# Performance work log

Measured on AMD Instinct MI355X. Metric: run time of the kernel, lower is better.

The kernel has to match this reference:

```python
import jax, jax.numpy as jnp
import numpy as np

B, C, H, W = 16, 512, 32, 32
G = 32          # GroupNorm groups
EPS = 1e-5      # torch GroupNorm default eps


def setup_inputs() -> dict:
    key = jax.random.key(0)
    ks = jax.random.split(key, 7)
    s = 0.02
    return {
        "x": jax.random.normal(ks[0], (B, C, H, W), jnp.float32),
        "temb": jax.random.normal(ks[1], (1, C), jnp.float32),
        "gn_scale": jnp.ones((C,), jnp.float32),
        "gn_bias": jnp.zeros((C,), jnp.float32),
        "wq": jax.random.normal(ks[2], (C, C), jnp.float32) * s,
        "bq": jnp.zeros((C,), jnp.float32),
        "wk": jax.random.normal(ks[3], (C, C), jnp.float32) * s,
        "bk": jnp.zeros((C,), jnp.float32),
        "wv": jax.random.normal(ks[4], (C, C), jnp.float32) * s,
        "bv": jnp.zeros((C,), jnp.float32),
        "wo": jax.random.normal(ks[5], (C, C), jnp.float32) * s,
        "bo": jnp.zeros((C,), jnp.float32),
    }


def _group_norm(x, scale, bias):
    b, c, h, w = x.shape
    xg = x.reshape(b, G, c // G, h, w)
    mu = xg.mean(axis=(2, 3, 4), keepdims=True)
    var = xg.var(axis=(2, 3, 4), keepdims=True)
    xn = ((xg - mu) * jax.lax.rsqrt(var + EPS)).reshape(b, c, h, w)
    return xn * scale[None, :, None, None] + bias[None, :, None, None]


def _conv1x1(x, w, b):
    # 1x1 conv == channel matmul
    return jnp.einsum('oc,bchw->bohw', w, x) + b[None, :, None, None]


def reference(x, temb, gn_scale, gn_bias, wq, bq, wk, bk, wv, bv, wo, bo):
    b, c, h, w = x.shape
    hw = h * w
    hn = _group_norm(x, gn_scale, gn_bias)
    q = _conv1x1(hn, wq, bq).reshape(b, c, hw)   # (B, C, HW)
    k = _conv1x1(hn, wk, bk).reshape(b, c, hw)
    v = _conv1x1(hn, wv, bv).reshape(b, c, hw)
    # scores over spatial positions, scaled by C^-0.5
    attn = jnp.einsum('bci,bcj->bij', q, k) * (c ** -0.5)  # (B, HW, HW)
    attn = jax.nn.softmax(attn, axis=-1)
    out = jnp.einsum('bij,bcj->bci', attn, v).reshape(b, c, h, w)
    out = _conv1x1(out, wo, bo)
    return x + out
```

## Files before the change

kernel.cpp:

```cpp
#include <hip/hip_runtime.h>

#define B_   16
#define C_   512
#define HW_  1024
#define G_   32
#define CPG  16
#define EPS  1e-5f
#define CHW  ((size_t)C_ * HW_)
#define HW2  ((size_t)HW_ * HW_)

typedef __attribute__((ext_vector_type(8))) short bf16x8;
typedef __attribute__((ext_vector_type(4))) float f32x4;

__device__ inline unsigned short f2bf(float f) {
    union { float f; unsigned u; } v; v.f = f;
    unsigned r = v.u + 0x7fffu + ((v.u >> 16) & 1u);
    return (unsigned short)(r >> 16);
}
__device__ inline float bf2f(unsigned short h) {
    union { unsigned u; float f; } v; v.u = (unsigned)h << 16;
    return v.f;
}

__device__ inline void gload_lds16(const void* g, void* lds) {
    __builtin_amdgcn_global_load_lds(
        (const __attribute__((address_space(1))) void*)g,
        (__attribute__((address_space(3))) void*)lds,
        16, 0, 0);
}

__global__ __launch_bounds__(256) void prep_kernel(
    const float* __restrict__ w0, const float* __restrict__ w1,
    const float* __restrict__ w2, const float* __restrict__ w3,
    unsigned short* __restrict__ o0, unsigned short* __restrict__ o1,
    unsigned short* __restrict__ o2, unsigned short* __restrict__ o3,
    const float* __restrict__ bq, const float* __restrict__ bk,
    float* __restrict__ bqk)
{
    int id = blockIdx.x;
    if (id < 1024) {
        int wsel = id >> 8;
        int blk  = id & 255;
        const float* in = (wsel == 0) ? w0 : (wsel == 1) ? w1 : (wsel == 2) ? w2 : w3;
        unsigned short* out = (wsel == 0) ? o0 : (wsel == 1) ? o1 : (wsel == 2) ? o2 : o3;
        int i = (blk * 256 + threadIdx.x) * 4;
        float4 f = *reinterpret_cast<const float4*>(in + i);
        ushort4 o;
        o.x = f2bf(f.x); o.y = f2bf(f.y); o.z = f2bf(f.z); o.w = f2bf(f.w);
        *reinterpret_cast<ushort4*>(out + i) = o;
    } else {
        int t = threadIdx.x;
        bqk[t]       = bq[t];
        bqk[256 + t] = bq[256 + t];
        bqk[512 + t] = bk[t];
        bqk[768 + t] = bk[256 + t];
    }
}

__global__ __launch_bounds__(256) void gn_fused(
    const float* __restrict__ x, const float* __restrict__ scale,
    const float* __restrict__ bias, unsigned short* __restrict__ hn_g)
{
    const int bg = blockIdx.x;
    const int g  = bg & 31;
    const float* xp = x + (size_t)bg * CPG * HW_;
    const int N = CPG * HW_;

    float s = 0.f, ss = 0.f;
    const float4* xv = reinterpret_cast<const float4*>(xp);
#pragma unroll
    for (int k = 0; k < 16; ++k) {
        float4 v = xv[threadIdx.x + k * 256];
        s  += v.x + v.y + v.z + v.w;
        ss += v.x * v.x + v.y * v.y + v.z * v.z + v.w * v.w;
    }
    for (int off = 32; off; off >>= 1) {
        s  += __shfl_down(s,  off, 64);
        ss += __shfl_down(ss, off, 64);
    }
    __shared__ float red0[4], red1[4];
    int lane = threadIdx.x & 63, wid = threadIdx.x >> 6;
    if (lane == 0) { red0[wid] = s; red1[wid] = ss; }
    __syncthreads();
    __shared__ float smu, sinv;
    if (threadIdx.x == 0) {
        float S  = red0[0] + red0[1] + red0[2] + red0[3];
        float SS = red1[0] + red1[1] + red1[2] + red1[3];
        float mu = S / (float)N;
        float var = SS / (float)N - mu * mu;
        smu = mu; sinv = rsqrtf(var + EPS);
    }
    __syncthreads();
    const float mu = smu, inv = sinv;

    float scl[CPG], bia[CPG];
#pragma unroll
    for (int cc = 0; cc < CPG; ++cc) {
        float sc = scale[g * CPG + cc];
        scl[cc] = sc * inv;
        bia[cc] = bias[g * CPG + cc] - mu * sc * inv;
    }

    unsigned short* dst = hn_g + (size_t)bg * 16384;
#pragma unroll
    for (int it = 0; it < 4; ++it) {
        int i = it * 256 + threadIdx.x;
        __align__(16) unsigned short y[CPG];
#pragma unroll
        for (int cc = 0; cc < CPG; ++cc)
            y[cc] = f2bf(xp[cc * HW_ + i] * scl[cc] + bia[cc]);
        unsigned short* d = dst + (size_t)i * 16;
        *reinterpret_cast<uint4*>(d)     = *reinterpret_cast<uint4*>(&y[0]);
        *reinterpret_cast<uint4*>(d + 8) = *reinterpret_cast<uint4*>(&y[8]);
    }
}

template<int OUTF32, int BIASMODE, int HASRES, int GA, int GB>
__device__ __forceinline__ void gemm_body(
    short* lds, int bx, int by, int bz,
    const short* __restrict__ A, size_t sA, int ldA,
    const short* __restrict__ Bm, size_t sB, int ldB,
    void* __restrict__ Cm, size_t sC, int ldC,
    const float* __restrict__ bias,
    const float* __restrict__ res, size_t sR,
    int K, float alpha)
{
    const short* Ab = A  + (size_t)bz * sA;
    const short* Bb = Bm + (size_t)bz * sB;
    const int m0 = by * 128;
    const int n0 = bx * 128;

    const int t = threadIdx.x;
    const int wv = t >> 6, lane = t & 63;
    const int wm = wv >> 1, wn = wv & 1;
    const int fr = lane & 15;
    const int cb = (lane >> 4) * 16;

    size_t srcA0, srcA1, srcB0, srcB1;
    {
        int p0 = t * 16;
        int a0 = p0 ^ (((p0 >> 7) & 3) << 4);
        int p1 = 4096 + t * 16;
        int a1 = p1 ^ (((p1 >> 7) & 3) << 4);
        int r0 = a0 >> 6, cs0 = (a0 & 63) >> 1;
        int r1 = a1 >> 6, cs1 = (a1 & 63) >> 1;
        if (GA) {
            int mA0 = m0 + r0, mA1 = m0 + r1;
            srcA0 = (size_t)(mA0 >> 10) * 524288 + (size_t)(cs0 >> 4) * 16384
                  + (size_t)(mA0 & 1023) * 16 + (cs0 & 15);
            srcA1 = (size_t)(mA1 >> 10) * 524288 + (size_t)(cs1 >> 4) * 16384
                  + (size_t)(mA1 & 1023) * 16 + (cs1 & 15);
        } else {
            srcA0 = (size_t)(m0 + r0) * ldA + cs0;
            srcA1 = (size_t)(m0 + r1) * ldA + cs1;
        }
        if (GB) {
            int nB0 = n0 + r0, nB1 = n0 + r1;
            srcB0 = (size_t)(nB0 >> 10) * 524288 + (size_t)(cs0 >> 4) * 16384
                  + (size_t)(nB0 & 1023) * 16 + (cs0 & 15);
            srcB1 = (size_t)(nB1 >> 10) * 524288 + (size_t)(cs1 >> 4) * 16384
                  + (size_t)(nB1 & 1023) * 16 + (cs1 & 15);
        } else {
            srcB0 = (size_t)(n0 + r0) * ldB + cs0;
            srcB1 = (size_t)(n0 + r1) * ldB + cs1;
        }
    }
    auto stageA = [&](int par, int kh, int kt_src) {
        const size_t k0 = (size_t)(kt_src * 64 + kh * 32) * (GA ? 1024 : 1);
        const short* s = Ab + k0;
        short* d = &lds[(par * 2 + kh) * 4096 + t * 8];
        gload_lds16(s + srcA0, d);
        gload_lds16(s + srcA1, d + 2048);
    };
    auto stageB = [&](int par, int kh, int kt_src) {
        const size_t k0 = (size_t)(kt_src * 64 + kh * 32) * (GB ? 1024 : 1);
        const short* s = Bb + k0;
        short* d = &lds[16384 + (par * 2 + kh) * 4096 + t * 8];
        gload_lds16(s + srcB0, d);
        gload_lds16(s + srcB1, d + 2048);
    };

    int aoffs[4], boffs[4];
#pragma unroll
    for (int fi = 0; fi < 4; ++fi) {
        int row = wm * 64 + fi * 16 + fr;
        int off = row * 64 + cb;
        aoffs[fi] = off ^ (((off >> 7) & 3) << 4);
    }
#pragma unroll
    for (int fj = 0; fj < 4; ++fj) {
        int row = wn * 64 + fj * 16 + fr;
        int off = row * 64 + cb;
        boffs[fj] = off ^ (((off >> 7) & 3) << 4);
    }

    f32x4 acc[4][4];
#pragma unroll
    for (int i = 0; i < 4; ++i)
#pragma unroll
        for (int j = 0; j < 4; ++j) acc[i][j] = (f32x4){0.f, 0.f, 0.f, 0.f};

    const int NT = K >> 6;
    const char* L = (const char*)lds;

    stageA(0, 0, 0); stageB(0, 0, 0);
    stageA(0, 1, 0); stageB(0, 1, 0);
    stageA(1, 0, 1); stageB(1, 0, 1);

    for (int kt = 0; kt < NT; ++kt) {
        const int par = kt & 1;
        const int AB0 = (par * 2) * 8192;
        const int AB1 = AB0 + 8192;
        const int BB0 = 32768 + (par * 2) * 8192;
        const int BB1 = BB0 + 8192;

        bf16x8 af0, af1, af2, af3, bf0, bf1;

        if (kt == NT - 1) asm volatile("s_waitcnt vmcnt(4)\n\ts_barrier" ::: "memory");
        else              asm volatile("s_waitcnt vmcnt(8)\n\ts_barrier" ::: "memory");
        af0 = *(const bf16x8*)(L + AB0 + aoffs[0]);
        af1 = *(const bf16x8*)(L + AB0 + aoffs[1]);
        af2 = *(const bf16x8*)(L + AB0 + aoffs[2]);
        af3 = *(const bf16x8*)(L + AB0 + aoffs[3]);
        bf0 = *(const bf16x8*)(L + BB0 + boffs[0]);
        bf1 = *(const bf16x8*)(L + BB0 + boffs[1]);
        if (kt + 1 < NT) stageA(par ^ 1, 1, kt + 1);
        __builtin_amdgcn_s_setprio(1);
        acc[0][0] = __builtin_amdgcn_mfma_f32_16x16x32_bf16(af0, bf0, acc[0][0], 0, 0, 0);
        acc[1][0] = __builtin_amdgcn_mfma_f32_16x16x32_bf16(af1, bf0, acc[1][0], 0, 0, 0);
        acc[2][0] = __builtin_amdgcn_mfma_f32_16x16x32_bf16(af2, bf0, acc[2][0], 0, 0, 0);
        acc[3][0] = __builtin_amdgcn_mfma_f32_16x16x32_bf16(af3, bf0, acc[3][0], 0, 0, 0);
        acc[0][1] = __builtin_amdgcn_mfma_f32_16x16x32_bf16(af0, bf1, acc[0][1], 0, 0, 0);
        acc[1][1] = __builtin_amdgcn_mfma_f32_16x16x32_bf16(af1, bf1, acc[1][1], 0, 0, 0);
        acc[2][1] = __builtin_amdgcn_mfma_f32_16x16x32_bf16(af2, bf1, acc[2][1], 0, 0, 0);
        acc[3][1] = __builtin_amdgcn_mfma_f32_16x16x32_bf16(af3, bf1, acc[3][1], 0, 0, 0);
        __builtin_amdgcn_s_setprio(0);
        asm volatile("s_waitcnt lgkmcnt(0)\n\ts_barrier" ::: "memory");

        bf0 = *(const bf16x8*)(L + BB0 + boffs[2]);
        bf1 = *(const bf16x8*)(L + BB0 + boffs[3]);
        if (kt + 1 < NT) stageB(par ^ 1, 1, kt + 1);
        __builtin_amdgcn_s_setprio(1);
        acc[0][2] = __builtin_amdgcn_mfma_f32_16x16x32_bf16(af0, bf0, acc[0][2], 0, 0, 0);
        acc[1][2] = __builtin_amdgcn_mfma_f32_16x16x32_bf16(af1, bf0, acc[1][2], 0, 0, 0);
        acc[2][2] = __builtin_amdgcn_mfma_f32_16x16x32_bf16(af2, bf0, acc[2][2], 0, 0, 0);
        acc[3][2] = __builtin_amdgcn_mfma_f32_16x16x32_bf16(af3, bf0, acc[3][2], 0, 0, 0);
        acc[0][3] = __builtin_amdgcn_mfma_f32_16x16x32_bf16(af0, bf1, acc[0][3], 0, 0, 0);
        acc[1][3] = __builtin_amdgcn_mfma_f32_16x16x32_bf16(af1, bf1, acc[1][3], 0, 0, 0);
        acc[2][3] = __builtin_amdgcn_mfma_f32_16x16x32_bf16(af2, bf1, acc[2][3], 0, 0, 0);
        acc[3][3] = __builtin_amdgcn_mfma_f32_16x16x32_bf16(af3, bf1, acc[3][3], 0, 0, 0);
        __builtin_amdgcn_s_setprio(0);
        asm volatile("s_waitcnt lgkmcnt(0)\n\ts_barrier" ::: "memory");

        if (kt == NT - 1) asm volatile("s_waitcnt vmcnt(0)\n\ts_barrier" ::: "memory");
        else              asm volatile("s_waitcnt vmcnt(8)\n\ts_barrier" ::: "memory");
        af0 = *(const bf16x8*)(L + AB1 + aoffs[0]);
        af1 = *(const bf16x8*)(L + AB1 + aoffs[1]);
        af2 = *(const bf16x8*)(L + AB1 + aoffs[2]);
        af3 = *(const bf16x8*)(L + AB1 + aoffs[3]);
        bf0 = *(const bf16x8*)(L + BB1 + boffs[0]);
        bf1 = *(const bf16x8*)(L + BB1 + boffs[1]);
        if (kt + 2 < NT) stageA(par, 0, kt + 2);
        __builtin_amdgcn_s_setprio(1);
        acc[0][0] = __builtin_amdgcn_mfma_f32_16x16x32_bf16(af0, bf0, acc[0][0], 0, 0, 0);
        acc[1][0] = __builtin_amdgcn_mfma_f32_16x16x32_bf16(af1, bf0, acc[1][0], 0, 0, 0);
        acc[2][0] = __builtin_amdgcn_mfma_f32_16x16x32_bf16(af2, bf0, acc[2][0], 0, 0, 0);
        acc[3][0] = __builtin_amdgcn_mfma_f32_16x16x32_bf16(af3, bf0, acc[3][0], 0, 0, 0);
        acc[0][1] = __builtin_amdgcn_mfma_f32_16x16x32_bf16(af0, bf1, acc[0][1], 0, 0, 0);
        acc[1][1] = __builtin_amdgcn_mfma_f32_16x16x32_bf16(af1, bf1, acc[1][1], 0, 0, 0);
        acc[2][1] = __builtin_amdgcn_mfma_f32_16x16x32_bf16(af2, bf1, acc[2][1], 0, 0, 0);
        acc[3][1] = __builtin_amdgcn_mfma_f32_16x16x32_bf16(af3, bf1, acc[3][1], 0, 0, 0);
        __builtin_amdgcn_s_setprio(0);
        asm volatile("s_waitcnt lgkmcnt(0)\n\ts_barrier" ::: "memory");

        bf0 = *(const bf16x8*)(L + BB1 + boffs[2]);
        bf1 = *(const bf16x8*)(L + BB1 + boffs[3]);
        if (kt + 2 < NT) stageB(par, 0, kt + 2);
        __builtin_amdgcn_s_setprio(1);
        acc[0][2] = __builtin_amdgcn_mfma_f32_16x16x32_bf16(af0, bf0, acc[0][2], 0, 0, 0);
        acc[1][2] = __builtin_amdgcn_mfma_f32_16x16x32_bf16(af1, bf0, acc[1][2], 0, 0, 0);
        acc[2][2] = __builtin_amdgcn_mfma_f32_16x16x32_bf16(af2, bf0, acc[2][2], 0, 0, 0);
        acc[3][2] = __builtin_amdgcn_mfma_f32_16x16x32_bf16(af3, bf0, acc[3][2], 0, 0, 0);
        acc[0][3] = __builtin_amdgcn_mfma_f32_16x16x32_bf16(af0, bf1, acc[0][3], 0, 0, 0);
        acc[1][3] = __builtin_amdgcn_mfma_f32_16x16x32_bf16(af1, bf1, acc[1][3], 0, 0, 0);
        acc[2][3] = __builtin_amdgcn_mfma_f32_16x16x32_bf16(af2, bf1, acc[2][3], 0, 0, 0);
        acc[3][3] = __builtin_amdgcn_mfma_f32_16x16x32_bf16(af3, bf1, acc[3][3], 0, 0, 0);
        __builtin_amdgcn_s_setprio(0);
        asm volatile("s_waitcnt lgkmcnt(0)\n\ts_barrier" ::: "memory");
    }

    const int rq = (lane >> 4) * 4;
#pragma unroll
    for (int fi = 0; fi < 4; ++fi) {
#pragma unroll
        for (int rg = 0; rg < 4; ++rg) {
            int row = m0 + wm * 64 + fi * 16 + rq + rg;
            float bm = (BIASMODE == 1) ? bias[row] : 0.f;
#pragma unroll
            for (int fj = 0; fj < 4; ++fj) {
                int col = n0 + wn * 64 + fj * 16 + fr;
                float vv = acc[fi][fj][rg] * alpha + bm;
                if (BIASMODE == 2) vv += bias[col];
                size_t off = (size_t)row * ldC + col;
                if (HASRES) vv += res[(size_t)bz * sR + off];
                if (OUTF32) ((float*)Cm)[(size_t)bz * sC + off] = vv;
                else ((unsigned short*)Cm)[(size_t)bz * sC + off] = f2bf(vv);
            }
        }
    }
}

template<int OUTF32, int BIASMODE, int HASRES, int GA, int GB>
__global__ __launch_bounds__(256) void gemm_4w(
    const short* __restrict__ A, size_t sA, int ldA,
    const short* __restrict__ Bm, size_t sB, int ldB,
    void* __restrict__ Cm, size_t sC, int ldC,
    const float* __restrict__ bias,
    const float* __restrict__ res, size_t sR,
    int K, float alpha, int lx, int ly)
{
    __shared__ __align__(16) short lds[32768];
    const int h = blockIdx.x;
    const int w = (h & 7) * ((int)gridDim.x >> 3) + (h >> 3);
    const int bx = w & ((1 << lx) - 1);
    const int by = (w >> lx) & ((1 << ly) - 1);
    const int bz = w >> (lx + ly);
    gemm_body<OUTF32, BIASMODE, HASRES, GA, GB>(
        lds, bx, by, bz, A, sA, ldA, Bm, sB, ldB, Cm, sC, ldC,
        bias, res, sR, K, alpha);
}

__global__ __launch_bounds__(256) void qkv_kernel(
    const short* __restrict__ hn_g, const short* __restrict__ wsq,
    const float* __restrict__ bqk, short* __restrict__ qk_t,
    const short* __restrict__ wsv, const float* __restrict__ bv,
    short* __restrict__ v)
{
    __shared__ __align__(16) short lds[32768];
    const int h = blockIdx.x;
    const int w = (h & 7) * 192 + (h >> 3);
    if (w < 1024) {
        gemm_body<0, 2, 0, 1, 0>(lds, w & 7, w >> 3, 0,
            hn_g, 0, 0, wsq, 0, C_, qk_t, 0, HW_, bqk, nullptr, 0, C_, 1.0f);
    } else {
        const int u = w - 1024;
        gemm_body<0, 1, 0, 0, 1>(lds, u & 7, (u >> 3) & 3, u >> 5,
            wsv, 0, C_, hn_g, CHW, 0, v, CHW, HW_, bv, nullptr, 0, C_, 1.0f);
    }
}

__global__ __launch_bounds__(256) void softmax_kernel(unsigned short* __restrict__ attn)
{
    size_t row = blockIdx.x;
    unsigned short* p = attn + row * HW_;
    ushort4 raw = reinterpret_cast<ushort4*>(p)[threadIdx.x];
    float v0 = bf2f(raw.x), v1 = bf2f(raw.y), v2 = bf2f(raw.z), v3 = bf2f(raw.w);

    float mx = fmaxf(fmaxf(v0, v1), fmaxf(v2, v3));
    for (int off = 32; off; off >>= 1) mx = fmaxf(mx, __shfl_down(mx, off, 64));
    __shared__ float redm[4], reds[4];
    int lane = threadIdx.x & 63, wid = threadIdx.x >> 6;
    if (lane == 0) redm[wid] = mx;
    __syncthreads();
    mx = fmaxf(fmaxf(redm[0], redm[1]), fmaxf(redm[2], redm[3]));

    v0 = __expf(v0 - mx); v1 = __expf(v1 - mx);
    v2 = __expf(v2 - mx); v3 = __expf(v3 - mx);
    float sum = v0 + v1 + v2 + v3;
    for (int off = 32; off; off >>= 1) sum += __shfl_down(sum, off, 64);
    if (lane == 0) reds[wid] = sum;
    __syncthreads();
    sum = reds[0] + reds[1] + reds[2] + reds[3];

    float inv = 1.f / sum;
    ushort4 o;
    o.x = f2bf(v0 * inv); o.y = f2bf(v1 * inv);
    o.z = f2bf(v2 * inv); o.w = f2bf(v3 * inv);
    reinterpret_cast<ushort4*>(p)[threadIdx.x] = o;
}

extern "C" void kernel_launch(void* const* d_in, const int* in_sizes, int n_in,
                              void* d_out, int out_size, void* d_ws, size_t ws_size,
                              hipStream_t stream)
{
    const float* x        = (const float*)d_in[0];
    const float* gn_scale = (const float*)d_in[2];
    const float* gn_bias  = (const float*)d_in[3];
    const float* wq = (const float*)d_in[4];
    const float* bq = (const float*)d_in[5];
    const float* wk = (const float*)d_in[6];
    const float* bk = (const float*)d_in[7];
    const float* wv = (const float*)d_in[8];
    const float* bv = (const float*)d_in[9];
    const float* wo = (const float*)d_in[10];
    const float* bo = (const float*)d_in[11];
    float* out = (float*)d_out;

    short* ws = (short*)d_ws;
    const size_t E = (size_t)B_ * C_ * HW_;
    short* hn_g = ws;
    short* qk_t = hn_g + E;
    short* v    = qk_t + 2 * E;
    short* ao_t = v + E;
    short* attn = ao_t + E;
    short* wsq  = attn + 2 * E;
    short* wsk  = wsq + (size_t)C_ * C_;
    short* wsv  = wsk + (size_t)C_ * C_;
    short* wso  = wsv + (size_t)C_ * C_;
    float* bqk  = (float*)(wso + (size_t)C_ * C_);

    const float inv_sqrt_c = 0.044194173824159216f;

    prep_kernel<<<dim3(1025), 256, 0, stream>>>(
        wq, wk, wv, wo,
        (unsigned short*)wsq, (unsigned short*)wsk,
        (unsigned short*)wsv, (unsigned short*)wso,
        bq, bk, bqk);

    gn_fused<<<dim3(B_ * G_), 256, 0, stream>>>(
        x, gn_scale, gn_bias, (unsigned short*)hn_g);

    qkv_kernel<<<dim3(1536), 256, 0, stream>>>(
        hn_g, wsq, bqk, qk_t, wsv, bv, v);

    gemm_4w<0, 0, 0, 0, 0><<<dim3(1024), 256, 0, stream>>>(
        qk_t, HW2, HW_, qk_t + C_, HW2, HW_, attn, HW2, HW_,
        nullptr, nullptr, 0, C_, inv_sqrt_c, 3, 3);

    softmax_kernel<<<dim3(B_ * HW_), 256, 0, stream>>>((unsigned short*)attn);

    gemm_4w<0, 0, 0, 0, 0><<<dim3(512), 256, 0, stream>>>(
        attn, HW2, HW_, v, CHW, HW_, ao_t, CHW, C_,
        nullptr, nullptr, 0, HW_, 1.0f, 2, 3);

    gemm_4w<1, 1, 1, 0, 0><<<dim3(512), 256, 0, stream>>>(
        wso, 0, C_, ao_t, CHW, C_, out, CHW, HW_, bo, x, CHW, C_,
        1.0f, 3, 2);
}
```

Before: 132.9 us.

## Fuse softmax normalization into PV GEMM A-tile load via precomputed row stats

Replaces the in-place softmax kernel with a stats-only pass that writes per-row max and inverse sum. The attention-times-V GEMM then loads raw scores into registers, applies exp and normalization, and writes bf16 to LDS, instead of staging the tile with direct global-to-LDS copies. This removes the softmax write-back of the full score matrix. In exchange the GEMM's A path now goes through registers with exp work inside the main loop, and the pipeline wait counts are retuned, which may reduce overlap.

```diff
diff --git a/kernel.cpp b/kernel.cpp
--- a/kernel.cpp
+++ b/kernel.cpp
@@ -115,7 +115,34 @@
     }
 }
 
-template<int OUTF32, int BIASMODE, int HASRES, int GA, int GB>
+__global__ __launch_bounds__(256) void row_stats(const unsigned short* __restrict__ attn,
+                                                 float2* __restrict__ rowstat)
+{
+    const int h = blockIdx.x;
+    const int row = (h & 7) * 2048 + (h >> 3);
+    const unsigned short* p = attn + (size_t)row * HW_;
+    ushort4 raw = reinterpret_cast<const ushort4*>(p)[threadIdx.x];
+    float v0 = bf2f(raw.x), v1 = bf2f(raw.y), v2 = bf2f(raw.z), v3 = bf2f(raw.w);
+
+    float mx = fmaxf(fmaxf(v0, v1), fmaxf(v2, v3));
+    for (int off = 32; off; off >>= 1) mx = fmaxf(mx, __shfl_down(mx, off, 64));
+    __shared__ float redm[4], reds[4];
+    int lane = threadIdx.x & 63, wid = threadIdx.x >> 6;
+    if (lane == 0) redm[wid] = mx;
+    __syncthreads();
+    mx = fmaxf(fmaxf(redm[0], redm[1]), fmaxf(redm[2], redm[3]));
+
+    float sum = __expf(v0 - mx) + __expf(v1 - mx) + __expf(v2 - mx) + __expf(v3 - mx);
+    for (int off = 32; off; off >>= 1) sum += __shfl_down(sum, off, 64);
+    if (lane == 0) reds[wid] = sum;
+    __syncthreads();
+    if (threadIdx.x == 0) {
+        float l = reds[0] + reds[1] + reds[2] + reds[3];
+        rowstat[row] = make_float2(mx, 1.0f / l);
+    }
+}
+
+template<int OUTF32, int BIASMODE, int HASRES, int GA, int GB, int AEXP>
 __device__ __forceinline__ void gemm_body(
     short* lds, int bx, int by, int bz,
     const short* __restrict__ A, size_t sA, int ldA,
@@ -123,7 +150,7 @@
     void* __restrict__ Cm, size_t sC, int ldC,
     const float* __restrict__ bias,
     const float* __restrict__ res, size_t sR,
-    int K, float alpha)
+    int K, float alpha, const float2* __restrict__ rowstat)
 {
     const short* Ab = A  + (size_t)bz * sA;
     const short* Bb = Bm + (size_t)bz * sB;
@@ -137,6 +164,7 @@
     const int cb = (lane >> 4) * 16;
 
     size_t srcA0, srcA1, srcB0, srcB1;
+    int rowA0, rowA1;
     {
         int p0 = t * 16;
         int a0 = p0 ^ (((p0 >> 7) & 3) << 4);
@@ -144,6 +172,7 @@
         int a1 = p1 ^ (((p1 >> 7) & 3) << 4);
         int r0 = a0 >> 6, cs0 = (a0 & 63) >> 1;
         int r1 = a1 >> 6, cs1 = (a1 & 63) >> 1;
+        rowA0 = r0; rowA1 = r1;
         if (GA) {
             int mA0 = m0 + r0, mA1 = m0 + r1;
             srcA0 = (size_t)(mA0 >> 10) * 524288 + (size_t)(cs0 >> 4) * 16384
@@ -180,6 +209,31 @@
         gload_lds16(s + srcB1, d + 2048);
     };
 
+    float msA0 = 0.f, ilA0 = 0.f, msA1 = 0.f, ilA1 = 0.f;
+    if (AEXP) {
+        float2 r0 = rowstat[bz * 1024 + m0 + rowA0];
+        float2 r1 = rowstat[bz * 1024 + m0 + rowA1];
+        msA0 = r0.x; ilA0 = r0.y; msA1 = r1.x; ilA1 = r1.y;
+    }
+    auto loadA2 = [&](int kh, int kt_src, bf16x8& c0, bf16x8& c1) {
+        const short* s = Ab + kt_src * 64 + kh * 32;
+        c0 = *(const bf16x8*)(s + srcA0);
+        c1 = *(const bf16x8*)(s + srcA1);
+    };
+    auto procA = [&](int par, int kh, bf16x8 c0, bf16x8 c1) {
+        short* d = &lds[(par * 2 + kh) * 4096 + t * 8];
+        bf16x8 o0, o1;
+#pragma unroll
+        for (int e = 0; e < 8; ++e) {
+            float q0 = __expf(bf2f((unsigned short)c0[e]) - msA0) * ilA0;
+            float q1 = __expf(bf2f((unsigned short)c1[e]) - msA1) * ilA1;
+            o0[e] = (short)f2bf(q0);
+            o1[e] = (short)f2bf(q1);
+        }
+        *(bf16x8*)d = o0;
+        *(bf16x8*)(d + 2048) = o1;
+    };
+
     int aoffs[4], boffs[4];
 #pragma unroll
     for (int fi = 0; fi < 4; ++fi) {
@@ -203,9 +257,27 @@
     const int NT = K >> 6;
     const char* L = (const char*)lds;
 
-    stageA(0, 0, 0); stageB(0, 0, 0);
-    stageA(0, 1, 0); stageB(0, 1, 0);
-    stageA(1, 0, 1); stageB(1, 0, 1);
+    bf16x8 cK0a, cK0b, cK1a, cK1b;
+
+    if (AEXP) {
+        bf16x8 t0a, t0b, t0c, t0d;
+        loadA2(0, 0, t0a, t0b);
+        asm volatile("" ::: "memory");
+        loadA2(1, 0, t0c, t0d);
+        asm volatile("" ::: "memory");
+        stageB(0, 0, 0); stageB(0, 1, 0); stageB(1, 0, 1);
+        asm volatile("" ::: "memory");
+        procA(0, 0, t0a, t0b);
+        procA(0, 1, t0c, t0d);
+        loadA2(0, 1, cK0a, cK0b);
+        asm volatile("" ::: "memory");
+        loadA2(1, 1, cK1a, cK1b);
+        asm volatile("s_waitcnt lgkmcnt(0)" ::: "memory");
+    } else {
+        stageA(0, 0, 0); stageB(0, 0, 0);
+        stageA(0, 1, 0); stageB(0, 1, 0);
+        stageA(1, 0, 1); stageB(1, 0, 1);
+    }
 
     for (int kt = 0; kt < NT; ++kt) {
         const int par = kt & 1;
@@ -216,15 +288,25 @@
 
         bf16x8 af0, af1, af2, af3, bf0, bf1;
 
-        if (kt == NT - 1) asm volatile("s_waitcnt vmcnt(4)\n\ts_barrier" ::: "memory");
-        else              asm volatile("s_waitcnt vmcnt(8)\n\ts_barrier" ::: "memory");
+        if (AEXP) {
+            if (kt == NT - 1) asm volatile("s_waitcnt vmcnt(2)\n\ts_barrier" ::: "memory");
+            else              asm volatile("s_waitcnt vmcnt(6)\n\ts_barrier" ::: "memory");
+        } else {
+            if (kt == NT - 1) asm volatile("s_waitcnt vmcnt(4)\n\ts_barrier" ::: "memory");
+            else              asm volatile("s_waitcnt vmcnt(8)\n\ts_barrier" ::: "memory");
+        }
         af0 = *(const bf16x8*)(L + AB0 + aoffs[0]);
         af1 = *(const bf16x8*)(L + AB0 + aoffs[1]);
         af2 = *(const bf16x8*)(L + AB0 + aoffs[2]);
         af3 = *(const bf16x8*)(L + AB0 + aoffs[3]);
         bf0 = *(const bf16x8*)(L + BB0 + boffs[0]);
         bf1 = *(const bf16x8*)(L + BB0 + boffs[1]);
-        if (kt + 1 < NT) stageA(par ^ 1, 1, kt + 1);
+        if (AEXP) {
+            if (kt + 1 < NT) procA(par ^ 1, 0, cK0a, cK0b);
+            if (kt + 2 < NT) loadA2(0, kt + 2, cK0a, cK0b);
+        } else {
+            if (kt + 1 < NT) stageA(par ^ 1, 1, kt + 1);
+        }
         __builtin_amdgcn_s_setprio(1);
         acc[0][0] = __builtin_amdgcn_mfma_f32_16x16x32_bf16(af0, bf0, acc[0][0], 0, 0, 0);
         acc[1][0] = __builtin_amdgcn_mfma_f32_16x16x32_bf16(af1, bf0, acc[1][0], 0, 0, 0);
@@ -252,15 +334,26 @@
         __builtin_amdgcn_s_setprio(0);
         asm volatile("s_waitcnt lgkmcnt(0)\n\ts_barrier" ::: "memory");
 
-        if (kt == NT - 1) asm volatile("s_waitcnt vmcnt(0)\n\ts_barrier" ::: "memory");
-        else              asm volatile("s_waitcnt vmcnt(8)\n\ts_barrier" ::: "memory");
+        if (AEXP) {
+            if (kt == NT - 1)      asm volatile("s_waitcnt vmcnt(0)\n\ts_barrier" ::: "memory");
+            else if (kt == NT - 2) asm volatile("s_waitcnt vmcnt(4)\n\ts_barrier" ::: "memory");
+            else                   asm volatile("s_waitcnt vmcnt(6)\n\ts_barrier" ::: "memory");
+        } else {
+            if (kt == NT - 1) asm volatile("s_waitcnt vmcnt(0)\n\ts_barrier" ::: "memory");
+            else              asm volatile("s_waitcnt vmcnt(8)\n\ts_barrier" ::: "memory");
+        }
         af0 = *(const bf16x8*)(L + AB1 + aoffs[0]);
         af1 = *(const bf16x8*)(L + AB1 + aoffs[1]);
         af2 = *(const bf16x8*)(L + AB1 + aoffs[2]);
         af3 = *(const bf16x8*)(L + AB1 + aoffs[3]);
         bf0 = *(const bf16x8*)(L + BB1 + boffs[0]);
         bf1 = *(const bf16x8*)(L + BB1 + boffs[1]);
-        if (kt + 2 < NT) stageA(par, 0, kt + 2);
+        if (AEXP) {
+            if (kt + 1 < NT) procA(par ^ 1, 1, cK1a, cK1b);
+            if (kt + 2 < NT) loadA2(1, kt + 2, cK1a, cK1b);
+        } else {
+            if (kt + 2 < NT) stageA(par, 0, kt + 2);
+        }
         __builtin_amdgcn_s_setprio(1);
         acc[0][0] = __builtin_amdgcn_mfma_f32_16x16x32_bf16(af0, bf0, acc[0][0], 0, 0, 0);
         acc[1][0] = __builtin_amdgcn_mfma_f32_16x16x32_bf16(af1, bf0, acc[1][0], 0, 0, 0);
@@ -310,14 +403,14 @@
     }
 }
 
-template<int OUTF32, int BIASMODE, int HASRES, int GA, int GB>
+template<int OUTF32, int BIASMODE, int HASRES, int GA, int GB, int AEXP>
 __global__ __launch_bounds__(256) void gemm_4w(
     const short* __restrict__ A, size_t sA, int ldA,
     const short* __restrict__ Bm, size_t sB, int ldB,
     void* __restrict__ Cm, size_t sC, int ldC,
     const float* __restrict__ bias,
     const float* __restrict__ res, size_t sR,
-    int K, float alpha, int lx, int ly)
+    int K, float alpha, int lx, int ly, const float2* rowstat)
 {
     __shared__ __align__(16) short lds[32768];
     const int h = blockIdx.x;
@@ -325,9 +418,9 @@
     const int bx = w & ((1 << lx) - 1);
     const int by = (w >> lx) & ((1 << ly) - 1);
     const int bz = w >> (lx + ly);
-    gemm_body<OUTF32, BIASMODE, HASRES, GA, GB>(
+    gemm_body<OUTF32, BIASMODE, HASRES, GA, GB, AEXP>(
         lds, bx, by, bz, A, sA, ldA, Bm, sB, ldB, Cm, sC, ldC,
-        bias, res, sR, K, alpha);
+        bias, res, sR, K, alpha, rowstat);
 }
 
 __global__ __launch_bounds__(256) void qkv_kernel(
@@ -340,43 +433,13 @@
     const int h = blockIdx.x;
     const int w = (h & 7) * 192 + (h >> 3);
     if (w < 1024) {
-        gemm_body<0, 2, 0, 1, 0>(lds, w & 7, w >> 3, 0,
-            hn_g, 0, 0, wsq, 0, C_, qk_t, 0, HW_, bqk, nullptr, 0, C_, 1.0f);
+        gemm_body<0, 2, 0, 1, 0, 0>(lds, w & 7, w >> 3, 0,
+            hn_g, 0, 0, wsq, 0, C_, qk_t, 0, HW_, bqk, nullptr, 0, C_, 1.0f, nullptr);
     } else {
         const int u = w - 1024;
-        gemm_body<0, 1, 0, 0, 1>(lds, u & 7, (u >> 3) & 3, u >> 5,
-            wsv, 0, C_, hn_g, CHW, 0, v, CHW, HW_, bv, nullptr, 0, C_, 1.0f);
-    }
-}
-
-__global__ __launch_bounds__(256) void softmax_kernel(unsigned short* __restrict__ attn)
-{
-    size_t row = blockIdx.x;
-    unsigned short* p = attn + row * HW_;
-    ushort4 raw = reinterpret_cast<ushort4*>(p)[threadIdx.x];
-    float v0 = bf2f(raw.x), v1 = bf2f(raw.y), v2 = bf2f(raw.z), v3 = bf2f(raw.w);
-
-    float mx = fmaxf(fmaxf(v0, v1), fmaxf(v2, v3));
-    for (int off = 32; off; off >>= 1) mx = fmaxf(mx, __shfl_down(mx, off, 64));
-    __shared__ float redm[4], reds[4];
-    int lane = threadIdx.x & 63, wid = threadIdx.x >> 6;
-    if (lane == 0) redm[wid] = mx;
-    __syncthreads();
-    mx = fmaxf(fmaxf(redm[0], redm[1]), fmaxf(redm[2], redm[3]));
-
-    v0 = __expf(v0 - mx); v1 = __expf(v1 - mx);
-    v2 = __expf(v2 - mx); v3 = __expf(v3 - mx);
-    float sum = v0 + v1 + v2 + v3;
-    for (int off = 32; off; off >>= 1) sum += __shfl_down(sum, off, 64);
-    if (lane == 0) reds[wid] = sum;
-    __syncthreads();
-    sum = reds[0] + reds[1] + reds[2] + reds[3];
-
-    float inv = 1.f / sum;
-    ushort4 o;
-    o.x = f2bf(v0 * inv); o.y = f2bf(v1 * inv);
-    o.z = f2bf(v2 * inv); o.w = f2bf(v3 * inv);
-    reinterpret_cast<ushort4*>(p)[threadIdx.x] = o;
+        gemm_body<0, 1, 0, 0, 1, 0>(lds, u & 7, (u >> 3) & 3, u >> 5,
+            wsv, 0, C_, hn_g, CHW, 0, v, CHW, HW_, bv, nullptr, 0, C_, 1.0f, nullptr);
+    }
 }
 
 extern "C" void kernel_launch(void* const* d_in, const int* in_sizes, int n_in,
@@ -408,6 +471,7 @@
     short* wsv  = wsk + (size_t)C_ * C_;
     short* wso  = wsv + (size_t)C_ * C_;
     float* bqk  = (float*)(wso + (size_t)C_ * C_);
+    float2* rowstat = (float2*)(bqk + 1024);
 
     const float inv_sqrt_c = 0.044194173824159216f;
 
@@ -423,17 +487,17 @@
     qkv_kernel<<<dim3(1536), 256, 0, stream>>>(
         hn_g, wsq, bqk, qk_t, wsv, bv, v);
 
-    gemm_4w<0, 0, 0, 0, 0><<<dim3(1024), 256, 0, stream>>>(
+    gemm_4w<0, 0, 0, 0, 0, 0><<<dim3(1024), 256, 0, stream>>>(
         qk_t, HW2, HW_, qk_t + C_, HW2, HW_, attn, HW2, HW_,
-        nullptr, nullptr, 0, C_, inv_sqrt_c, 3, 3);
-
-    softmax_kernel<<<dim3(B_ * HW_), 256, 0, stream>>>((unsigned short*)attn);
-
-    gemm_4w<0, 0, 0, 0, 0><<<dim3(512), 256, 0, stream>>>(
+        nullptr, nullptr, 0, C_, inv_sqrt_c, 3, 3, nullptr);
+
+    row_stats<<<dim3(B_ * HW_), 256, 0, stream>>>((unsigned short*)attn, rowstat);
+
+    gemm_4w<0, 0, 0, 0, 0, 1><<<dim3(512), 256, 0, stream>>>(
         attn, HW2, HW_, v, CHW, HW_, ao_t, CHW, C_,
-        nullptr, nullptr, 0, HW_, 1.0f, 2, 3);
-
-    gemm_4w<1, 1, 1, 0, 0><<<dim3(512), 256, 0, stream>>>(
+        nullptr, nullptr, 0, HW_, 1.0f, 2, 3, rowstat);
+
+    gemm_4w<1, 1, 1, 0, 0, 0><<<dim3(512), 256, 0, stream>>>(
         wso, 0, C_, ao_t, CHW, C_, out, CHW, HW_, bo, x, CHW, C_,
-        1.0f, 3, 2);
-}
+        1.0f, 3, 2, nullptr);
+}
```

Result: slower. 141.1 us (+6.1%).
